# Optimization experiments

Measured on AMD Instinct MI355X. Metric: run time of the kernel, lower is better.

The kernel has to match this reference:

```python
import jax, jax.numpy as jnp
import numpy as np

U, I, D = 100000, 50000, 64       # users, items, latdim
H, DH = 4, 16                      # att_head, head dim (D = H*DH)
HN = 128                           # hyperNum
L = 2                              # hgnn_layer
HOPS = 2                           # gcn_hops
SLOPE = 0.5                        # leaky
NNZ_UI = 1000000
NNZ_UU = 1000000


def leaky(x):
    return jnp.where(x >= 0, x, SLOPE * x)


def spmm(rows, cols, vals, X, n_out):
    # sparse COO @ dense: out[r] += vals * X[c]
    return jax.ops.segment_sum(vals[:, None] * X[cols], rows, num_segments=n_out)


def lightgcn(uE, iE, ar, ac, av, tr, tc, tv):
    ulats, ilats = [uE], [iE]
    for _ in range(HOPS):
        tu = spmm(ar, ac, av, ilats[-1], U)
        ti = spmm(tr, tc, tv, ulats[-1], I)
        ulats.append(tu)
        ilats.append(ti)
    return sum(ulats[1:]), sum(ilats[1:])


def lightgcn2(uE, ur, uc, uv):
    lats = [uE]
    for _ in range(HOPS):
        lats.append(spmm(ur, uc, uv, lats[-1], U))
    return sum(lats[1:])


def prepare_key(E, K):
    # [N, D] -> [H, N, DH]
    return (E @ K).reshape(-1, H, DH).transpose(1, 0, 2)


def hg_transformer(E0, Key, Hyper, V, pV, W1, W2):
    # Hyper: [HN, D]; Key: [H, N, DH]
    hyp = Hyper.reshape(HN, H, DH).transpose(1, 2, 0)  # [H, DH, HN]
    total = E0
    cur = E0
    for l in range(L):
        value = (cur @ pV).reshape(-1, H, DH).transpose(1, 2, 0)   # [H, DH, N]
        t1 = ((value @ Key) @ hyp).reshape(D, HN)                  # [D, HN]
        t2 = leaky(t1 @ W1[l].T) + t1                              # Linear(HN,HN) no bias
        t3 = leaky(t2 @ W2[l].T) + t2
        pre = (t3.T @ V).reshape(HN, H, DH).transpose(1, 0, 2)     # [H, HN, DH]
        pre = hyp @ pre                                            # [H, DH, DH]
        new = (Key @ pre).transpose(1, 0, 2).reshape(-1, D)        # [N, D]
        total = total + new
        cur = new
    return total, Hyper


def setup_inputs() -> dict:
    key = jax.random.key(0)
    ks = jax.random.split(key, 14)
    s = 0.05
    uEmbeds0 = jax.random.normal(ks[0], (U, D), jnp.float32) * s
    iEmbeds0 = jax.random.normal(ks[1], (I, D), jnp.float32) * s
    Ks = jax.random.normal(ks[2], (3, D, D), jnp.float32) * (1.0 / np.sqrt(D))
    hg_Hyper = jax.random.normal(ks[3], (3, HN, D), jnp.float32) * s
    hg_V = jax.random.normal(ks[4], (3, D, D), jnp.float32) * (1.0 / np.sqrt(D))
    hg_pV = jax.random.normal(ks[5], (3, D, D), jnp.float32) * (1.0 / np.sqrt(D))
    hg_W1 = jax.random.normal(ks[6], (3, L, HN, HN), jnp.float32) * (1.0 / np.sqrt(HN))
    hg_W2 = jax.random.normal(ks[7], (3, L, HN, HN), jnp.float32) * (1.0 / np.sqrt(HN))
    adj_rows = jax.random.randint(ks[8], (NNZ_UI,), 0, U, jnp.int32)
    adj_cols = jax.random.randint(ks[9], (NNZ_UI,), 0, I, jnp.int32)
    adj_vals = jax.random.uniform(ks[10], (NNZ_UI,), jnp.float32)
    uu_rows = jax.random.randint(ks[11], (NNZ_UU,), 0, U, jnp.int32)
    uu_cols = jax.random.randint(ks[12], (NNZ_UU,), 0, U, jnp.int32)
    uu_vals = jax.random.uniform(ks[13], (NNZ_UU,), jnp.float32)
    return dict(uEmbeds0=uEmbeds0, iEmbeds0=iEmbeds0, Ks=Ks, hg_Hyper=hg_Hyper,
                hg_V=hg_V, hg_pV=hg_pV, hg_W1=hg_W1, hg_W2=hg_W2,
                adj_rows=adj_rows, adj_cols=adj_cols, adj_vals=adj_vals,
                tp_rows=adj_cols, tp_cols=adj_rows, tp_vals=adj_vals,
                uu_rows=uu_rows, uu_cols=uu_cols, uu_vals=uu_vals)


def reference(uEmbeds0, iEmbeds0, Ks, hg_Hyper, hg_V, hg_pV, hg_W1, hg_W2,
              adj_vals, tp_vals, uu_vals,
              adj_rows, adj_cols, tp_rows, tp_cols, uu_rows, uu_cols):
    ui_u_gcn, ui_i_gcn = lightgcn(uEmbeds0, iEmbeds0, adj_rows, adj_cols, adj_vals,
                                  tp_rows, tp_cols, tp_vals)
    uu_gcn = lightgcn2(uEmbeds0, uu_rows, uu_cols, uu_vals)
    ui_uEmbed0 = uEmbeds0 + ui_u_gcn
    ui_iEmbed0 = iEmbeds0 + ui_i_gcn
    uu_Embed0 = uEmbeds0 + uu_gcn
    ui_uKey = prepare_key(ui_uEmbed0, Ks[0])
    ui_iKey = prepare_key(ui_iEmbed0, Ks[1])
    uu_Key = prepare_key(uu_Embed0, Ks[2])
    ui_ulat, ui_uHyper = hg_transformer(ui_uEmbed0, ui_uKey, hg_Hyper[0], hg_V[0], hg_pV[0], hg_W1[0], hg_W2[0])
    ui_ilat, ui_iHyper = hg_transformer(ui_iEmbed0, ui_iKey, hg_Hyper[1], hg_V[1], hg_pV[1], hg_W1[1], hg_W2[1])
    uu_lat, uu_Hyper = hg_transformer(uu_Embed0, uu_Key, hg_Hyper[2], hg_V[2], hg_pV[2], hg_W1[2], hg_W2[2])
    return (ui_uEmbed0, ui_iEmbed0, ui_ulat, ui_ilat, ui_uKey, ui_iKey,
            ui_uHyper, ui_iHyper, uu_Embed0, uu_lat, uu_Key, uu_Hyper)
```

## Files before the change

### kernel.cpp

```cpp
#include <hip/hip_runtime.h>

#define ATB_B 256

__global__ __launch_bounds__(256) void hist3(const int* __restrict__ rA,
                                             const int* __restrict__ rT,
                                             const int* __restrict__ rU,
                                             int nnzA, int nnzU,
                                             int* __restrict__ cntAll, int U, int I) {
    int i = blockIdx.x * 256 + threadIdx.x;
    int tot = 2 * nnzA + nnzU;
    if (i >= tot) return;
    if (i < nnzA) atomicAdd(&cntAll[rA[i]], 1);
    else if (i < 2 * nnzA) atomicAdd(&cntAll[U + rT[i - nnzA]], 1);
    else atomicAdd(&cntAll[U + I + rU[i - 2 * nnzA]], 1);
}

__global__ __launch_bounds__(256) void scan_part3(const int* __restrict__ cntAll,
                                                  int* __restrict__ bsumAll,
                                                  int U, int I, int nbA, int nbT) {
    int b = blockIdx.x;
    int lb, n, coff, bsoff;
    if (b < nbA)            { lb = b;             n = U; coff = 0;     bsoff = 0; }
    else if (b < nbA + nbT) { lb = b - nbA;       n = I; coff = U;     bsoff = 1024; }
    else                    { lb = b - nbA - nbT; n = U; coff = U + I; bsoff = 2048; }
    __shared__ int sh[256];
    int tid = threadIdx.x;
    int i = lb * 256 + tid;
    sh[tid] = (i < n) ? cntAll[coff + i] : 0;
    __syncthreads();
    for (int st = 128; st > 0; st >>= 1) {
        if (tid < st) sh[tid] += sh[tid + st];
        __syncthreads();
    }
    if (tid == 0) bsumAll[bsoff + lb] = sh[0];
}

__global__ __launch_bounds__(1024) void scan_top3(int* __restrict__ bsumAll,
                                                  int nbA, int nbT, int nbU) {
    int g = blockIdx.x;
    int nb = (g == 0) ? nbA : (g == 1 ? nbT : nbU);
    int* b = bsumAll + g * 1024;
    __shared__ int sh[1024];
    int tid = threadIdx.x;
    int orig = (tid < nb) ? b[tid] : 0;
    sh[tid] = orig;
    __syncthreads();
    for (int st = 1; st < 1024; st <<= 1) {
        int v = (tid >= st) ? sh[tid - st] : 0;
        __syncthreads();
        sh[tid] += v;
        __syncthreads();
    }
    if (tid < nb) b[tid] = sh[tid] - orig;
}

__global__ __launch_bounds__(256) void scan_final3(int* __restrict__ curAll,
                                                   const int* __restrict__ bsumAll,
                                                   int* __restrict__ rpAll,
                                                   int U, int I, int nbA, int nbT,
                                                   int nnzA, int nnzU) {
    int b = blockIdx.x;
    int lb, n, coff, bsoff, rpoff, nnz;
    if (b < nbA)            { lb = b;             n = U; coff = 0;     bsoff = 0;    rpoff = 0;                 nnz = nnzA; }
    else if (b < nbA + nbT) { lb = b - nbA;       n = I; coff = U;     bsoff = 1024; rpoff = U + 1;             nnz = nnzA; }
    else                    { lb = b - nbA - nbT; n = U; coff = U + I; bsoff = 2048; rpoff = (U + 1) + (I + 1); nnz = nnzU; }
    __shared__ int sh[256];
    int tid = threadIdx.x;
    int i = lb * 256 + tid;
    int orig = (i < n) ? curAll[coff + i] : 0;
    sh[tid] = orig;
    __syncthreads();
    for (int st = 1; st < 256; st <<= 1) {
        int v = (tid >= st) ? sh[tid - st] : 0;
        __syncthreads();
        sh[tid] += v;
        __syncthreads();
    }
    int ex = sh[tid] - orig + bsumAll[bsoff + lb];
    if (i < n) { rpAll[rpoff + i] = ex; curAll[coff + i] = ex; }
    if (i == n - 1) rpAll[rpoff + n] = nnz;
}

__global__ __launch_bounds__(256) void scatter3(const int* __restrict__ rA, const int* __restrict__ cA, const float* __restrict__ vA,
                                                const int* __restrict__ rT, const int* __restrict__ cT, const float* __restrict__ vT,
                                                const int* __restrict__ rU, const int* __restrict__ cU, const float* __restrict__ vU,
                                                int* __restrict__ curAll, int2* __restrict__ eAll,
                                                int nnzA, int nnzU, int U, int I) {
    int i = blockIdx.x * 256 + threadIdx.x;
    int tot = 2 * nnzA + nnzU;
    if (i >= tot) return;
    if (i < nnzA) {
        int p = atomicAdd(&curAll[rA[i]], 1);
        eAll[p] = make_int2(cA[i], __float_as_int(vA[i]));
    } else if (i < 2 * nnzA) {
        int j = i - nnzA;
        int p = atomicAdd(&curAll[U + rT[j]], 1);
        eAll[nnzA + p] = make_int2(cT[j], __float_as_int(vT[j]));
    } else {
        int j = i - 2 * nnzA;
        int p = atomicAdd(&curAll[U + I + rU[j]], 1);
        eAll[2 * nnzA + p] = make_int2(cU[j], __float_as_int(vU[j]));
    }
}

struct Seg { const int* rp; const int2* eg; const float* X; const float* a0; const float* a1; float* out; int N; };
struct Spmm3Args { Seg s0, s1, s2; int n0, n01, total; };

__global__ __launch_bounds__(256) void spmm3(Spmm3Args A) {
    int gid = blockIdx.x * 256 + threadIdx.x;
    int r = gid >> 6;
    if (r >= A.total) return;
    int d = gid & 63;
    Seg sg; int lr;
    if (r < A.n0)       { sg = A.s0; lr = r; }
    else if (r < A.n01) { sg = A.s1; lr = r - A.n0; }
    else                { sg = A.s2; lr = r - A.n01; }
    int s = sg.rp[lr], e = sg.rp[lr + 1];
    const float* __restrict__ X = sg.X;
    float acc = 0.f;
    int i = s;
    for (; i + 4 <= e; i += 4) {
        int2 e0 = sg.eg[i], e1 = sg.eg[i + 1], e2 = sg.eg[i + 2], e3 = sg.eg[i + 3];
        float x0 = X[(size_t)e0.x * 64 + d];
        float x1 = X[(size_t)e1.x * 64 + d];
        float x2 = X[(size_t)e2.x * 64 + d];
        float x3 = X[(size_t)e3.x * 64 + d];
        acc += __int_as_float(e0.y) * x0;
        acc += __int_as_float(e1.y) * x1;
        acc += __int_as_float(e2.y) * x2;
        acc += __int_as_float(e3.y) * x3;
    }
    for (; i < e; ++i) {
        int2 ee = sg.eg[i];
        acc += __int_as_float(ee.y) * X[(size_t)ee.x * 64 + d];
    }
    size_t o = (size_t)lr * 64 + d;
    if (sg.a0) acc += sg.a0[o];
    if (sg.a1) acc += sg.a1[o];
    sg.out[o] = acc;
}

struct KSeg { const float* E; const float* K; float* Kout; int N; };
struct Key3Args { KSeg s0, s1, s2; int b1, b2; };

__global__ __launch_bounds__(256) void key3(Key3Args A) {
    int b = blockIdx.x;
    KSeg sg; int lb;
    if (b >= A.b2)      { sg = A.s2; lb = b - A.b2; }
    else if (b >= A.b1) { sg = A.s1; lb = b - A.b1; }
    else                { sg = A.s0; lb = b; }
    __shared__ float Ksh[4096];
    int tid = threadIdx.x;
    for (int i = tid; i < 4096; i += 256) Ksh[i] = sg.K[i];
    __syncthreads();
    int j = tid & 63, slot = tid >> 6;
    int n = lb * 4 + slot;
    if (n >= sg.N) return;
    const float* Er = sg.E + (size_t)n * 64;
    float acc = 0.f;
#pragma unroll
    for (int kk = 0; kk < 64; ++kk) acc += Er[kk] * Ksh[kk * 64 + j];
    int h = j >> 4, dh = j & 15;
    sg.Kout[((size_t)h * sg.N + n) * 16 + dh] = acc;
}

__global__ __launch_bounds__(256) void atb3(const float* __restrict__ c0, const float* __restrict__ c1, const float* __restrict__ c2,
                                            const float* __restrict__ K0, const float* __restrict__ K1, const float* __restrict__ K2,
                                            int N0, int N1, int N2,
                                            float* __restrict__ part) {
    int kidx = blockIdx.x / ATB_B;
    int lb = blockIdx.x % ATB_B;
    const float* cur = (kidx == 0) ? c0 : (kidx == 1 ? c1 : c2);
    const float* Key = (kidx == 0) ? K0 : (kidx == 1 ? K1 : K2);
    int N = (kidx == 0) ? N0 : (kidx == 1 ? N1 : N2);
    int chunk = (N + ATB_B - 1) / ATB_B;
    int tid = threadIdx.x;
    int k = tid & 63, h = tid >> 6;
    const float* Kh = Key + (size_t)h * N * 16;
    float acc[16];
#pragma unroll
    for (int i = 0; i < 16; ++i) acc[i] = 0.f;
    int s = lb * chunk;
    int e = s + chunk;
    if (e > N) e = N;
#pragma unroll 2
    for (int n = s; n < e; ++n) {
        float c = cur[(size_t)n * 64 + k];
        const float4* kr = (const float4*)(Kh + (size_t)n * 16);
        float4 k0 = kr[0], k1 = kr[1], k2 = kr[2], k3 = kr[3];
        acc[0]  += c * k0.x;  acc[1]  += c * k0.y;  acc[2]  += c * k0.z;  acc[3]  += c * k0.w;
        acc[4]  += c * k1.x;  acc[5]  += c * k1.y;  acc[6]  += c * k1.z;  acc[7]  += c * k1.w;
        acc[8]  += c * k2.x;  acc[9]  += c * k2.y;  acc[10] += c * k2.z;  acc[11] += c * k2.w;
        acc[12] += c * k3.x;  acc[13] += c * k3.y;  acc[14] += c * k3.z;  acc[15] += c * k3.w;
    }
    float4* po = (float4*)(part + ((size_t)kidx * ATB_B + lb) * 4096 + k * 64 + h * 16);
    po[0] = make_float4(acc[0],  acc[1],  acc[2],  acc[3]);
    po[1] = make_float4(acc[4],  acc[5],  acc[6],  acc[7]);
    po[2] = make_float4(acc[8],  acc[9],  acc[10], acc[11]);
    po[3] = make_float4(acc[12], acc[13], acc[14], acc[15]);
}

__global__ __launch_bounds__(256) void reduce3(const float* __restrict__ part,
                                               float* __restrict__ Mall) {
    int k = blockIdx.x >> 4;
    int i = (blockIdx.x & 15) * 256 + threadIdx.x;
    const float* p = part + (size_t)k * ATB_B * 4096 + i;
    float s = 0.f;
#pragma unroll 8
    for (int b = 0; b < ATB_B; ++b) s += p[(size_t)b * 4096];
    Mall[k * 4096 + i] = s;
}

__global__ __launch_bounds__(1024) void chain3(const float* __restrict__ Mall,
                                               const float* __restrict__ pV,
                                               const float* __restrict__ hyp3,
                                               const float* __restrict__ W1,
                                               const float* __restrict__ W2,
                                               const float* __restrict__ Vt,
                                               float* __restrict__ pre2all, int l) {
    int kg = blockIdx.x;
    const float* M    = Mall + kg * 4096;
    const float* pVk  = pV + kg * 4096;
    const float* hyp  = hyp3 + kg * 8192;
    const float* W1kl = W1 + (size_t)(kg * 2 + l) * 16384;
    const float* W2kl = W2 + (size_t)(kg * 2 + l) * 16384;
    const float* Vk   = Vt + kg * 4096;
    float* pre2 = pre2all + kg * 1024;

    __shared__ float tA[8192];
    __shared__ float tB[8192];
    __shared__ float hypsh[8192];
    __shared__ float shW[64 * 129 + 64];
    __shared__ float VKs[1024];

    int tid = threadIdx.x;
    for (int i = tid; i < 8192; i += 1024) hypsh[i] = hyp[i];
    for (int i = tid; i < 4096; i += 1024) { shW[i] = M[i]; shW[4096 + i] = pVk[i]; }
    __syncthreads();

    {
        int d2 = tid & 15, d1 = (tid >> 4) & 15, h = tid >> 8;
        float s = 0.f;
#pragma unroll
        for (int k2 = 0; k2 < 64; ++k2)
            s += shW[4096 + k2 * 64 + h * 16 + d1] * shW[k2 * 64 + h * 16 + d2];
        VKs[tid] = s;
    }
    __syncthreads();

    for (int i = tid; i < 8192; i += 1024) {
        int m = i & 127, d = i >> 7, h = d >> 4;
        float s = 0.f;
#pragma unroll
        for (int d2 = 0; d2 < 16; ++d2) s += VKs[d * 16 + d2] * hypsh[(h * 16 + d2) * 128 + m];
        tA[i] = s;
    }
    __syncthreads();

    {
        float acc[8];
#pragma unroll
        for (int j = 0; j < 8; ++j) acc[j] = 0.f;
        for (int c = 0; c < 2; ++c) {
            __syncthreads();
            for (int t = tid; t < 8192; t += 1024) {
                int m = t >> 6, mml = t & 63;
                shW[mml * 129 + m] = W1kl[m * 128 + c * 64 + mml];
            }
            __syncthreads();
#pragma unroll
            for (int j = 0; j < 8; ++j) {
                int i = tid + j * 1024;
                int m = i & 127, d = i >> 7;
                const float* tr = tA + d * 128 + c * 64;
                float s = 0.f;
#pragma unroll
                for (int mm = 0; mm < 64; ++mm) s += tr[mm] * shW[mm * 129 + m];
                acc[j] += s;
            }
        }
#pragma unroll
        for (int j = 0; j < 8; ++j) {
            int i = tid + j * 1024;
            float s = acc[j];
            tB[i] = (s >= 0.f ? s : 0.5f * s) + tA[i];
        }
    }
    __syncthreads();

    {
        float acc[8];
#pragma unroll
        for (int j = 0; j < 8; ++j) acc[j] = 0.f;
        for (int c = 0; c < 2; ++c) {
            __syncthreads();
            for (int t = tid; t < 8192; t += 1024) {
                int m = t >> 6, mml = t & 63;
                shW[mml * 129 + m] = W2kl[m * 128 + c * 64 + mml];
            }
            __syncthreads();
#pragma unroll
            for (int j = 0; j < 8; ++j) {
                int i = tid + j * 1024;
                int m = i & 127, d = i >> 7;
                const float* tr = tB + d * 128 + c * 64;
                float s = 0.f;
#pragma unroll
                for (int mm = 0; mm < 64; ++mm) s += tr[mm] * shW[mm * 129 + m];
                acc[j] += s;
            }
        }
#pragma unroll
        for (int j = 0; j < 8; ++j) {
            int i = tid + j * 1024;
            float s = acc[j];
            tA[i] = (s >= 0.f ? s : 0.5f * s) + tB[i];
        }
    }
    __syncthreads();

    for (int i = tid; i < 4096; i += 1024) shW[i] = Vk[i];
    __syncthreads();

    for (int i = tid; i < 8192; i += 1024) {
        int dd = i & 63, m = i >> 6;
        float s = 0.f;
#pragma unroll
        for (int d = 0; d < 64; ++d) s += tA[d * 128 + m] * shW[d * 64 + dd];
        tB[i] = s;
    }
    __syncthreads();

    {
        int d2 = tid & 15, d1 = (tid >> 4) & 15, h = tid >> 8;
        float s = 0.f;
#pragma unroll
        for (int m = 0; m < 128; ++m)
            s += hypsh[(h * 16 + d1) * 128 + m] * tB[m * 64 + h * 16 + d2];
        pre2[tid] = s;
    }
}

struct ESeg { const float* Key; const float* pre2; const float* in; float* out1; float* out2; int N; };
struct Exp3Args { ESeg s0, s1, s2; int b1, b2; };

__global__ __launch_bounds__(256) void expand3(Exp3Args A, int mode) {
    int b = blockIdx.x;
    ESeg sg; int lb;
    if (b >= A.b2)      { sg = A.s2; lb = b - A.b2; }
    else if (b >= A.b1) { sg = A.s1; lb = b - A.b1; }
    else                { sg = A.s0; lb = b; }
    __shared__ float p2[1024];
    int tid = threadIdx.x;
    for (int i = tid; i < 1024; i += 256) p2[i] = sg.pre2[i];
    __syncthreads();
    int j = tid & 63, slot = tid >> 6;
    int n = lb * 4 + slot;
    if (n >= sg.N) return;
    int h = j >> 4, d2 = j & 15;
    const float* kr = sg.Key + ((size_t)h * sg.N + n) * 16;
    float s = 0.f;
#pragma unroll
    for (int d1 = 0; d1 < 16; ++d1) s += kr[d1] * p2[(h * 16 + d1) * 16 + d2];
    size_t o = (size_t)n * 64 + j;
    if (mode == 0) { sg.out1[o] = s; sg.out2[o] = sg.in[o] + s; }
    else           { sg.out1[o] = sg.in[o] + s; }
}

__global__ __launch_bounds__(256) void hyp_kernel(const float* __restrict__ Hyper,
                                                  float* __restrict__ hyp3,
                                                  float* __restrict__ out,
                                                  size_t off0, size_t off1, size_t off2) {
    int i = blockIdx.x * 256 + threadIdx.x;
    if (i >= 3 * 8192) return;
    int k = i / 8192, r = i % 8192;
    float v = Hyper[i];
    size_t off = (k == 0) ? off0 : ((k == 1) ? off1 : off2);
    out[off + r] = v;
    int m = r >> 6, dcol = r & 63;
    hyp3[k * 8192 + dcol * 128 + m] = v;
}

__global__ __launch_bounds__(256) void spmm_k(const int* __restrict__ rows,
                                              const int* __restrict__ cols,
                                              const float* __restrict__ vals,
                                              const float* __restrict__ X,
                                              float* __restrict__ out, int nnz) {
    int gid = blockIdx.x * 256 + threadIdx.x;
    int e = gid >> 6;
    if (e >= nnz) return;
    int d = gid & 63;
    int r = rows[e], c = cols[e];
    float v = vals[e];
    atomicAdd(&out[(size_t)r * 64 + d], v * X[(size_t)c * 64 + d]);
}

__global__ __launch_bounds__(256) void add3_kernel(const float* __restrict__ base,
                                                   const float* __restrict__ a,
                                                   const float* __restrict__ b,
                                                   float* __restrict__ outb, size_t n) {
    size_t i = (size_t)blockIdx.x * 256 + threadIdx.x;
    if (i >= n) return;
    outb[i] = base[i] + a[i] + b[i];
}

__global__ __launch_bounds__(256) void key_gemm(const float* __restrict__ E,
                                                const float* __restrict__ K,
                                                float* __restrict__ Kout, int N) {
    __shared__ float Ksh[4096];
    int tid = threadIdx.x;
    for (int i = tid; i < 4096; i += 256) Ksh[i] = K[i];
    __syncthreads();
    int j = tid & 63, slot = tid >> 6;
    int n = blockIdx.x * 4 + slot;
    if (n >= N) return;
    const float* Er = E + (size_t)n * 64;
    float acc = 0.f;
#pragma unroll
    for (int kk = 0; kk < 64; ++kk) acc += Er[kk] * Ksh[kk * 64 + j];
    int h = j >> 4, dh = j & 15;
    Kout[((size_t)h * N + n) * 16 + dh] = acc;
}

#define ATB_ROWS 128
__global__ __launch_bounds__(256) void atb_k(const float* __restrict__ cur,
                                             const float* __restrict__ Key,
                                             float* __restrict__ M, int N) {
    int tid = threadIdx.x;
    int k = tid & 63, h = tid >> 6;
    const float* Kh = Key + (size_t)h * N * 16;
    float acc[16];
#pragma unroll
    for (int i = 0; i < 16; ++i) acc[i] = 0.f;
    int s = blockIdx.x * ATB_ROWS;
    int e = s + ATB_ROWS;
    if (e > N) e = N;
    for (int n = s; n < e; ++n) {
        float c = cur[(size_t)n * 64 + k];
        const float4* kr = (const float4*)(Kh + (size_t)n * 16);
        float4 k0 = kr[0], k1 = kr[1], k2 = kr[2], k3 = kr[3];
        acc[0]  += c * k0.x;  acc[1]  += c * k0.y;  acc[2]  += c * k0.z;  acc[3]  += c * k0.w;
        acc[4]  += c * k1.x;  acc[5]  += c * k1.y;  acc[6]  += c * k1.z;  acc[7]  += c * k1.w;
        acc[8]  += c * k2.x;  acc[9]  += c * k2.y;  acc[10] += c * k2.z;  acc[11] += c * k2.w;
        acc[12] += c * k3.x;  acc[13] += c * k3.y;  acc[14] += c * k3.z;  acc[15] += c * k3.w;
    }
#pragma unroll
    for (int d2 = 0; d2 < 16; ++d2)
        atomicAdd(&M[k * 64 + h * 16 + d2], acc[d2]);
}

__global__ __launch_bounds__(256) void vk_small(const float* __restrict__ M,
                                                const float* __restrict__ pV,
                                                float* __restrict__ VK) {
    int i = blockIdx.x * 256 + threadIdx.x;
    if (i >= 1024) return;
    int d2 = i & 15, d1 = (i >> 4) & 15, h = i >> 8;
    float s = 0.f;
#pragma unroll
    for (int k = 0; k < 64; ++k)
        s += pV[k * 64 + h * 16 + d1] * M[k * 64 + h * 16 + d2];
    VK[i] = s;
}

__global__ __launch_bounds__(256) void t1_kernel(const float* __restrict__ VK,
                                                 const float* __restrict__ hyp,
                                                 float* __restrict__ t1) {
    int i = blockIdx.x * 256 + threadIdx.x;
    if (i >= 8192) return;
    int m = i & 127, d = i >> 7, h = d >> 4;
    float s = 0.f;
#pragma unroll
    for (int d2 = 0; d2 < 16; ++d2) s += VK[d * 16 + d2] * hyp[(h * 16 + d2) * 128 + m];
    t1[i] = s;
}

__global__ __launch_bounds__(256) void ff_kernel(const float* __restrict__ tin,
                                                 const float* __restrict__ W,
                                                 float* __restrict__ tout) {
    int i = blockIdx.x * 256 + threadIdx.x;
    if (i >= 8192) return;
    int m = i & 127, d = i >> 7;
    const float* tr = tin + d * 128;
    const float* wr = W + m * 128;
    float s = 0.f;
#pragma unroll
    for (int mm = 0; mm < 128; ++mm) s += tr[mm] * wr[mm];
    tout[i] = (s >= 0.f ? s : 0.5f * s) + tin[i];
}

__global__ __launch_bounds__(256) void pre0_kernel(const float* __restrict__ t3,
                                                   const float* __restrict__ V,
                                                   float* __restrict__ pre0) {
    int i = blockIdx.x * 256 + threadIdx.x;
    if (i >= 8192) return;
    int dd = i & 63, m = i >> 6;
    float s = 0.f;
#pragma unroll
    for (int d = 0; d < 64; ++d) s += t3[d * 128 + m] * V[d * 64 + dd];
    pre0[m * 64 + dd] = s;
}

__global__ __launch_bounds__(256) void pre2_kernel(const float* __restrict__ hyp,
                                                   const float* __restrict__ pre0,
                                                   float* __restrict__ pre2) {
    int i = blockIdx.x * 256 + threadIdx.x;
    if (i >= 1024) return;
    int d2 = i & 15, d1 = (i >> 4) & 15, h = i >> 8;
    float s = 0.f;
#pragma unroll
    for (int m = 0; m < 128; ++m) s += hyp[(h * 16 + d1) * 128 + m] * pre0[m * 64 + h * 16 + d2];
    pre2[i] = s;
}

__global__ __launch_bounds__(256) void expand0_kernel(const float* __restrict__ Key,
                                                      const float* __restrict__ pre2,
                                                      const float* __restrict__ E0,
                                                      float* __restrict__ nxt,
                                                      float* __restrict__ tot, int N) {
    __shared__ float p2[1024];
    int tid = threadIdx.x;
    for (int i = tid; i < 1024; i += 256) p2[i] = pre2[i];
    __syncthreads();
    int j = tid & 63, slot = tid >> 6;
    int n = blockIdx.x * 4 + slot;
    if (n >= N) return;
    int h = j >> 4, d2 = j & 15;
    const float* kr = Key + ((size_t)h * N + n) * 16;
    float s = 0.f;
#pragma unroll
    for (int d1 = 0; d1 < 16; ++d1) s += kr[d1] * p2[(h * 16 + d1) * 16 + d2];
    size_t o = (size_t)n * 64 + j;
    nxt[o] = s;
    tot[o] = E0[o] + s;
}

__global__ __launch_bounds__(256) void expand1_kernel(const float* __restrict__ Key,
                                                      const float* __restrict__ pre2,
                                                      const float* __restrict__ tot,
                                                      float* __restrict__ outb, int N) {
    __shared__ float p2[1024];
    int tid = threadIdx.x;
    for (int i = tid; i < 1024; i += 256) p2[i] = pre2[i];
    __syncthreads();
    int j = tid & 63, slot = tid >> 6;
    int n = blockIdx.x * 4 + slot;
    if (n >= N) return;
    int h = j >> 4, d2 = j & 15;
    const float* kr = Key + ((size_t)h * N + n) * 16;
    float s = 0.f;
#pragma unroll
    for (int d1 = 0; d1 < 16; ++d1) s += kr[d1] * p2[(h * 16 + d1) * 16 + d2];
    size_t o = (size_t)n * 64 + j;
    outb[o] = tot[o] + s;
}

extern "C" void kernel_launch(void* const* d_in, const int* in_sizes, int n_in,
                              void* d_out, int out_size, void* d_ws, size_t ws_size,
                              hipStream_t stream) {
    const float* uE      = (const float*)d_in[0];
    const float* iE      = (const float*)d_in[1];
    const float* Ks      = (const float*)d_in[2];
    const float* Hyper   = (const float*)d_in[3];
    const float* Vt      = (const float*)d_in[4];
    const float* pV      = (const float*)d_in[5];
    const float* W1      = (const float*)d_in[6];
    const float* W2      = (const float*)d_in[7];
    const int* adj_rows  = (const int*)d_in[8];
    const int* adj_cols  = (const int*)d_in[9];
    const float* adj_vals= (const float*)d_in[10];
    const int* tp_rows   = (const int*)d_in[11];
    const int* tp_cols   = (const int*)d_in[12];
    const float* tp_vals = (const float*)d_in[13];
    const int* uu_rows   = (const int*)d_in[14];
    const int* uu_cols   = (const int*)d_in[15];
    const float* uu_vals = (const float*)d_in[16];

    const int U = in_sizes[0] / 64;
    const int I = in_sizes[1] / 64;
    const int nnz_ui = in_sizes[8];
    const int nnz_uu = in_sizes[14];
    const size_t UD = (size_t)U * 64, ID = (size_t)I * 64;

    float* out = (float*)d_out;
    const size_t o_uE0 = 0;
    const size_t o_iE0 = UD;
    const size_t o_ulat = UD + ID;
    const size_t o_ilat = 2 * UD + ID;
    const size_t o_uKey = 2 * UD + 2 * ID;
    const size_t o_iKey = 3 * UD + 2 * ID;
    const size_t o_uHyp = 3 * UD + 3 * ID;
    const size_t o_iHyp = o_uHyp + 8192;
    const size_t o_uuE0 = o_iHyp + 8192;
    const size_t o_uulat = o_uuE0 + UD;
    const size_t o_uuKey = o_uulat + UD;
    const size_t o_uuHyp = o_uuKey + UD;

    float* ws   = (float*)d_ws;
    float* B1   = ws;
    float* B2   = B1 + UD;
    float* B3   = B2 + ID;
    float* Ti   = B3 + UD;
    float* Buu1 = Ti + ID;
    float* Tuu  = Buu1 + UD;
    float* hyp3 = Tuu + UD;
    float* Mall = hyp3 + 24576;
    float* pre2all = Mall + 12288;
    int2*  edge_a = (int2*)(pre2all + 3072);
    int2*  edge_t = edge_a + nnz_ui;
    int2*  edge_u = edge_t + nnz_ui;
    int*   rpAll  = (int*)(edge_u + nnz_uu);
    int*   curAll = rpAll + (U + 1) + (I + 1) + (U + 1);
    int*   bsumAll= curAll + U + I + U;
    float* partw  = (float*)(bsumAll + 3072);
    size_t need_bytes = (size_t)((char*)(partw + (size_t)3 * ATB_B * 4096) - (char*)d_ws);
    const int nbA = (U + 255) / 256, nbT = (I + 255) / 256, nbU = (U + 255) / 256;
    const bool use_new = (ws_size >= need_bytes) && (nbA <= 1024) && (nbT <= 1024);

    int* rp_a = rpAll;
    int* rp_t = rpAll + (U + 1);
    int* rp_u = rpAll + (U + 1) + (I + 1);

    if (use_new) {
        hipMemsetAsync(curAll, 0, (size_t)(U + I + U) * sizeof(int), stream);
        int totE = 2 * nnz_ui + nnz_uu;
        hist3<<<(totE + 255) / 256, 256, 0, stream>>>(adj_rows, tp_rows, uu_rows,
                                                      nnz_ui, nnz_uu, curAll, U, I);
        scan_part3<<<nbA + nbT + nbU, 256, 0, stream>>>(curAll, bsumAll, U, I, nbA, nbT);
        scan_top3<<<3, 1024, 0, stream>>>(bsumAll, nbA, nbT, nbU);
        scan_final3<<<nbA + nbT + nbU, 256, 0, stream>>>(curAll, bsumAll, rpAll,
                                                         U, I, nbA, nbT, nnz_ui, nnz_uu);
        scatter3<<<(totE + 255) / 256, 256, 0, stream>>>(
            adj_rows, adj_cols, adj_vals, tp_rows, tp_cols, tp_vals,
            uu_rows, uu_cols, uu_vals, curAll, edge_a, nnz_ui, nnz_uu, U, I);

        {
            Spmm3Args A;
            A.s0 = { rp_t, edge_t, uE, nullptr, nullptr, B2, I };
            A.s1 = { rp_a, edge_a, iE, nullptr, nullptr, B1, U };
            A.s2 = { nullptr, nullptr, nullptr, nullptr, nullptr, nullptr, 0 };
            A.n0 = I; A.n01 = I + U; A.total = I + U;
            spmm3<<<(int)(((size_t)A.total * 64 + 255) / 256), 256, 0, stream>>>(A);
        }
        {
            Spmm3Args A;
            A.s0 = { rp_a, edge_a, B2, uE, B1, out + o_uE0, U };
            A.s1 = { rp_t, edge_t, B1, iE, B2, out + o_iE0, I };
            A.s2 = { rp_u, edge_u, uE, nullptr, nullptr, Buu1, U };
            A.n0 = U; A.n01 = U + I; A.total = U + I + U;
            spmm3<<<(int)(((size_t)A.total * 64 + 255) / 256), 256, 0, stream>>>(A);
        }
        {
            Spmm3Args A;
            A.s0 = { rp_u, edge_u, Buu1, uE, Buu1, out + o_uuE0, U };
            A.s1 = { nullptr, nullptr, nullptr, nullptr, nullptr, nullptr, 0 };
            A.s2 = A.s1;
            A.n0 = U; A.n01 = U; A.total = U;
            spmm3<<<(int)(((size_t)A.total * 64 + 255) / 256), 256, 0, stream>>>(A);
        }

        hyp_kernel<<<(3 * 8192 + 255) / 256, 256, 0, stream>>>(Hyper, hyp3, out,
                                                               o_uHyp, o_iHyp, o_uuHyp);

        const int gb0 = (U + 3) / 4, gb1 = (I + 3) / 4, gb2 = (U + 3) / 4;
        {
            Key3Args A;
            A.s0 = { out + o_uE0,  Ks,        out + o_uKey,  U };
            A.s1 = { out + o_iE0,  Ks + 4096, out + o_iKey,  I };
            A.s2 = { out + o_uuE0, Ks + 8192, out + o_uuKey, U };
            A.b1 = gb0; A.b2 = gb0 + gb1;
            key3<<<gb0 + gb1 + gb2, 256, 0, stream>>>(A);
        }

        const float* Key0 = out + o_uKey;
        const float* Key1 = out + o_iKey;
        const float* Key2 = out + o_uuKey;

        for (int l = 0; l < 2; ++l) {
            const float* c0 = (l == 0) ? (out + o_uE0)  : B1;
            const float* c1 = (l == 0) ? (out + o_iE0)  : B2;
            const float* c2 = (l == 0) ? (out + o_uuE0) : Buu1;

            atb3<<<3 * ATB_B, 256, 0, stream>>>(c0, c1, c2, Key0, Key1, Key2, U, I, U, partw);
            reduce3<<<48, 256, 0, stream>>>(partw, Mall);
            chain3<<<3, 1024, 0, stream>>>(Mall, pV, hyp3, W1, W2, Vt, pre2all, l);

            Exp3Args E;
            E.b1 = gb0; E.b2 = gb0 + gb1;
            if (l == 0) {
                E.s0 = { Key0, pre2all,        out + o_uE0,  B1,   B3,  U };
                E.s1 = { Key1, pre2all + 1024, out + o_iE0,  B2,   Ti,  I };
                E.s2 = { Key2, pre2all + 2048, out + o_uuE0, Buu1, Tuu, U };
                expand3<<<gb0 + gb1 + gb2, 256, 0, stream>>>(E, 0);
            } else {
                E.s0 = { Key0, pre2all,        B3,  out + o_ulat,  nullptr, U };
                E.s1 = { Key1, pre2all + 1024, Ti,  out + o_ilat,  nullptr, I };
                E.s2 = { Key2, pre2all + 2048, Tuu, out + o_uulat, nullptr, U };
                expand3<<<gb0 + gb1 + gb2, 256, 0, stream>>>(E, 1);
            }
        }
    } else {
        float* fB1 = ws;
        float* fB2 = fB1 + UD;
        float* fB3 = fB2 + ID;
        float* fhyp3 = fB2;
        float* fVK  = fhyp3 + 3 * 8192;
        float* ft1  = fVK + 1024;
        float* ft2  = ft1 + 8192;
        float* ft3  = ft2 + 8192;
        float* fpre0 = ft3 + 8192;
        float* fpre2 = fpre0 + 8192;
        float* fM   = fpre2 + 1024;

        const int g_ui = (int)(((size_t)nnz_ui * 64 + 255) / 256);
        const int g_uu = (int)(((size_t)nnz_uu * 64 + 255) / 256);
        const int gU = (int)((UD + 255) / 256);
        const int gI = (int)((ID + 255) / 256);
        hipMemsetAsync(fB1, 0, UD * sizeof(float), stream);
        spmm_k<<<g_ui, 256, 0, stream>>>(adj_rows, adj_cols, adj_vals, iE, fB1, nnz_ui);
        hipMemsetAsync(fB2, 0, ID * sizeof(float), stream);
        spmm_k<<<g_ui, 256, 0, stream>>>(tp_rows, tp_cols, tp_vals, uE, fB2, nnz_ui);
        hipMemsetAsync(fB3, 0, UD * sizeof(float), stream);
        spmm_k<<<g_ui, 256, 0, stream>>>(adj_rows, adj_cols, adj_vals, fB2, fB3, nnz_ui);
        add3_kernel<<<gU, 256, 0, stream>>>(uE, fB1, fB3, out + o_uE0, UD);
        hipMemsetAsync(fB3, 0, ID * sizeof(float), stream);
        spmm_k<<<g_ui, 256, 0, stream>>>(tp_rows, tp_cols, tp_vals, fB1, fB3, nnz_ui);
        add3_kernel<<<gI, 256, 0, stream>>>(iE, fB2, fB3, out + o_iE0, ID);
        hipMemsetAsync(fB1, 0, UD * sizeof(float), stream);
        spmm_k<<<g_uu, 256, 0, stream>>>(uu_rows, uu_cols, uu_vals, uE, fB1, nnz_uu);
        hipMemsetAsync(fB3, 0, UD * sizeof(float), stream);
        spmm_k<<<g_uu, 256, 0, stream>>>(uu_rows, uu_cols, uu_vals, fB1, fB3, nnz_uu);
        add3_kernel<<<gU, 256, 0, stream>>>(uE, fB1, fB3, out + o_uuE0, UD);

        hyp_kernel<<<(3 * 8192 + 255) / 256, 256, 0, stream>>>(Hyper, fhyp3, out,
                                                               o_uHyp, o_iHyp, o_uuHyp);

        const int    Narr[3] = { U, I, U };
        const size_t oE[3]   = { o_uE0, o_iE0, o_uuE0 };
        const size_t oK[3]   = { o_uKey, o_iKey, o_uuKey };
        const size_t oL[3]   = { o_ulat, o_ilat, o_uulat };

        for (int k = 0; k < 3; ++k) {
            int N = Narr[k];
            const float* E0k = out + oE[k];
            float* Keyk = out + oK[k];
            const float* Ksk = Ks + k * 4096;
            const float* pVk = pV + k * 4096;
            const float* Vk  = Vt + k * 4096;
            const float* hypk = fhyp3 + k * 8192;

            key_gemm<<<(N + 3) / 4, 256, 0, stream>>>(E0k, Ksk, Keyk, N);

            for (int l = 0; l < 2; ++l) {
                const float* W1kl = W1 + (size_t)(k * 2 + l) * 16384;
                const float* W2kl = W2 + (size_t)(k * 2 + l) * 16384;

                hipMemsetAsync(fM, 0, 4096 * sizeof(float), stream);
                atb_k<<<(N + ATB_ROWS - 1) / ATB_ROWS, 256, 0, stream>>>(
                    (l == 0) ? E0k : fB1, Keyk, fM, N);
                vk_small<<<4, 256, 0, stream>>>(fM, pVk, fVK);
                t1_kernel<<<32, 256, 0, stream>>>(fVK, hypk, ft1);
                ff_kernel<<<32, 256, 0, stream>>>(ft1, W1kl, ft2);
                ff_kernel<<<32, 256, 0, stream>>>(ft2, W2kl, ft3);
                pre0_kernel<<<32, 256, 0, stream>>>(ft3, Vk, fpre0);
                pre2_kernel<<<4, 256, 0, stream>>>(hypk, fpre0, fpre2);

                if (l == 0) {
                    expand0_kernel<<<(N + 3) / 4, 256, 0, stream>>>(Keyk, fpre2, E0k, fB1, fB3, N);
                } else {
                    expand1_kernel<<<(N + 3) / 4, 256, 0, stream>>>(Keyk, fpre2, fB3, out + oL[k], N);
                }
            }
        }
    }
}
```

Measured before the change: 1.705 ms.

## Build CSR with row-window LDS histograms and scatter instead of global atomics

Replaces the global-atomic COO histogram and scatter with kernels where each block owns an 8192-row window. Each block keeps counts and cursors in shared memory and streams the whole row array, keeping only rows in its window. This removes the global atomics and the memset. The cost is that every block rereads all nnz row indices: about 13+7+13 blocks each scan 1M entries. Only 33 blocks run, so GPU occupancy is very low.

Result: slower. 5.521 ms (+223.8%).

```diff
diff --git a/kernel.cpp b/kernel.cpp
--- a/kernel.cpp
+++ b/kernel.cpp
@@ -1,18 +1,32 @@
 #include <hip/hip_runtime.h>
 
 #define ATB_B 256
-
-__global__ __launch_bounds__(256) void hist3(const int* __restrict__ rA,
-                                             const int* __restrict__ rT,
-                                             const int* __restrict__ rU,
-                                             int nnzA, int nnzU,
-                                             int* __restrict__ cntAll, int U, int I) {
-    int i = blockIdx.x * 256 + threadIdx.x;
-    int tot = 2 * nnzA + nnzU;
-    if (i >= tot) return;
-    if (i < nnzA) atomicAdd(&cntAll[rA[i]], 1);
-    else if (i < 2 * nnzA) atomicAdd(&cntAll[U + rT[i - nnzA]], 1);
-    else atomicAdd(&cntAll[U + I + rU[i - 2 * nnzA]], 1);
+#define WROWS 8192
+
+__global__ __launch_bounds__(256) void hist_w(const int* __restrict__ rA,
+                                              const int* __restrict__ rT,
+                                              const int* __restrict__ rU,
+                                              int nnzA, int nnzU,
+                                              int* __restrict__ cntAll,
+                                              int U, int I, int wU, int wI) {
+    int b = blockIdx.x;
+    const int* rows; int nnz, n, coff, w;
+    if (b < wU)           { rows = rA; nnz = nnzA; n = U; coff = 0;     w = b; }
+    else if (b < wU + wI) { rows = rT; nnz = nnzA; n = I; coff = U;     w = b - wU; }
+    else                  { rows = rU; nnz = nnzU; n = U; coff = U + I; w = b - wU - wI; }
+    int w0 = w * WROWS;
+    int wend = w0 + WROWS; if (wend > n) wend = n;
+    int wlen = wend - w0;
+    __shared__ int cnt[WROWS];
+    int tid = threadIdx.x;
+    for (int i = tid; i < WROWS; i += 256) cnt[i] = 0;
+    __syncthreads();
+    for (int i = tid; i < nnz; i += 256) {
+        int r = rows[i];
+        if (r >= w0 && r < wend) atomicAdd(&cnt[r - w0], 1);
+    }
+    __syncthreads();
+    for (int i = tid; i < wlen; i += 256) cntAll[coff + w0 + i] = cnt[i];
 }
 
 __global__ __launch_bounds__(256) void scan_part3(const int* __restrict__ cntAll,
@@ -77,29 +91,34 @@
         __syncthreads();
     }
     int ex = sh[tid] - orig + bsumAll[bsoff + lb];
-    if (i < n) { rpAll[rpoff + i] = ex; curAll[coff + i] = ex; }
+    if (i < n) rpAll[rpoff + i] = ex;
     if (i == n - 1) rpAll[rpoff + n] = nnz;
 }
 
-__global__ __launch_bounds__(256) void scatter3(const int* __restrict__ rA, const int* __restrict__ cA, const float* __restrict__ vA,
-                                                const int* __restrict__ rT, const int* __restrict__ cT, const float* __restrict__ vT,
-                                                const int* __restrict__ rU, const int* __restrict__ cU, const float* __restrict__ vU,
-                                                int* __restrict__ curAll, int2* __restrict__ eAll,
-                                                int nnzA, int nnzU, int U, int I) {
-    int i = blockIdx.x * 256 + threadIdx.x;
-    int tot = 2 * nnzA + nnzU;
-    if (i >= tot) return;
-    if (i < nnzA) {
-        int p = atomicAdd(&curAll[rA[i]], 1);
-        eAll[p] = make_int2(cA[i], __float_as_int(vA[i]));
-    } else if (i < 2 * nnzA) {
-        int j = i - nnzA;
-        int p = atomicAdd(&curAll[U + rT[j]], 1);
-        eAll[nnzA + p] = make_int2(cT[j], __float_as_int(vT[j]));
-    } else {
-        int j = i - 2 * nnzA;
-        int p = atomicAdd(&curAll[U + I + rU[j]], 1);
-        eAll[2 * nnzA + p] = make_int2(cU[j], __float_as_int(vU[j]));
+__global__ __launch_bounds__(256) void scatter_w(const int* __restrict__ rA, const int* __restrict__ cA, const float* __restrict__ vA,
+                                                 const int* __restrict__ rT, const int* __restrict__ cT, const float* __restrict__ vT,
+                                                 const int* __restrict__ rU, const int* __restrict__ cU, const float* __restrict__ vU,
+                                                 const int* __restrict__ rpAll, int2* __restrict__ eAll,
+                                                 int nnzA, int nnzU, int U, int I, int wU, int wI) {
+    int b = blockIdx.x;
+    const int* rows; const int* cols; const float* vals;
+    int nnz, n, rpoff, w; size_t ebase;
+    if (b < wU)           { rows = rA; cols = cA; vals = vA; nnz = nnzA; n = U; rpoff = 0;                 ebase = 0;            w = b; }
+    else if (b < wU + wI) { rows = rT; cols = cT; vals = vT; nnz = nnzA; n = I; rpoff = U + 1;             ebase = nnzA;         w = b - wU; }
+    else                  { rows = rU; cols = cU; vals = vU; nnz = nnzU; n = U; rpoff = (U + 1) + (I + 1); ebase = 2 * (size_t)nnzA; w = b - wU - wI; }
+    int w0 = w * WROWS;
+    int wend = w0 + WROWS; if (wend > n) wend = n;
+    int wlen = wend - w0;
+    __shared__ int cur[WROWS];
+    int tid = threadIdx.x;
+    for (int i = tid; i < wlen; i += 256) cur[i] = rpAll[rpoff + w0 + i];
+    __syncthreads();
+    for (int i = tid; i < nnz; i += 256) {
+        int r = rows[i];
+        if (r >= w0 && r < wend) {
+            int p = atomicAdd(&cur[r - w0], 1);
+            eAll[ebase + p] = make_int2(cols[i], __float_as_int(vals[i]));
+        }
     }
 }
 
@@ -621,17 +640,17 @@
     int* rp_u = rpAll + (U + 1) + (I + 1);
 
     if (use_new) {
-        hipMemsetAsync(curAll, 0, (size_t)(U + I + U) * sizeof(int), stream);
-        int totE = 2 * nnz_ui + nnz_uu;
-        hist3<<<(totE + 255) / 256, 256, 0, stream>>>(adj_rows, tp_rows, uu_rows,
-                                                      nnz_ui, nnz_uu, curAll, U, I);
+        const int wU = (U + WROWS - 1) / WROWS;
+        const int wI = (I + WROWS - 1) / WROWS;
+        hist_w<<<wU + wI + wU, 256, 0, stream>>>(adj_rows, tp_rows, uu_rows,
+                                                 nnz_ui, nnz_uu, curAll, U, I, wU, wI);
         scan_part3<<<nbA + nbT + nbU, 256, 0, stream>>>(curAll, bsumAll, U, I, nbA, nbT);
         scan_top3<<<3, 1024, 0, stream>>>(bsumAll, nbA, nbT, nbU);
         scan_final3<<<nbA + nbT + nbU, 256, 0, stream>>>(curAll, bsumAll, rpAll,
                                                          U, I, nbA, nbT, nnz_ui, nnz_uu);
-        scatter3<<<(totE + 255) / 256, 256, 0, stream>>>(
+        scatter_w<<<wU + wI + wU, 256, 0, stream>>>(
             adj_rows, adj_cols, adj_vals, tp_rows, tp_cols, tp_vals,
-            uu_rows, uu_cols, uu_vals, curAll, edge_a, nnz_ui, nnz_uu, U, I);
+            uu_rows, uu_cols, uu_vals, rpAll, edge_a, nnz_ui, nnz_uu, U, I, wU, wI);
 
         {
             Spmm3Args A;
```
